# Optimization experiments

Measured on AMD Instinct MI355X. Metric: run time of the kernel, lower is better.

Reference implementation:

```python
import math
import jax, jax.numpy as jnp
import numpy as np

DIM = 2048
HEAD_DIM = 64
N_HEADS = DIM // HEAD_DIM
BATCH = 4
SEQ = 1025  # 32*32 axial positions + 1 zero position
EPS = 1e-6


def make_theta(head_dim=HEAD_DIM, h=32, w=32):
    # freqs: geometric from pi to 10*pi, head_dim//4 of them
    n_freqs = head_dim // 4
    freqs = jnp.exp(jnp.linspace(math.log(math.pi), math.log(10 * math.pi), n_freqs))
    hp = jnp.linspace(-1.0, 1.0, h + 1)
    wp = jnp.linspace(-1.0, 1.0, w + 1)
    hp = (hp[:-1] + hp[1:]) / 2
    wp = (wp[:-1] + wp[1:]) / 2
    pos = jnp.stack(jnp.meshgrid(hp, wp, indexing='ij'), axis=-1).reshape(h * w, 2)
    pos = jnp.concatenate([jnp.zeros((1, 2)), pos], axis=0)  # [1025, 2]
    theta_h = pos[:, 0:1] * freqs  # [S, n_freqs]
    theta_w = pos[:, 1:2] * freqs
    return jnp.concatenate([theta_h, theta_w], axis=-1)  # [S, head_dim//2]


def rms_norm(x, scale, eps=EPS):
    mean_sq = jnp.mean(jnp.square(x.astype(jnp.float32)), axis=-1, keepdims=True)
    s = scale.astype(jnp.float32) * jax.lax.rsqrt(mean_sq + eps)
    return (x * s.astype(x.dtype)).astype(x.dtype)


def apply_rotary(x, theta):
    # x: [B, H, S, D], theta: [S, d] with 2*d <= D
    d = theta.shape[-1]
    x1, x2, x3 = x[..., :d], x[..., d:2 * d], x[..., 2 * d:]
    cos, sin = jnp.cos(theta), jnp.sin(theta)  # broadcast over B, H
    y1 = x1 * cos - x2 * sin
    y2 = x2 * cos + x1 * sin
    return jnp.concatenate([y1, y2, x3], axis=-1)


def setup_inputs() -> dict:
    key = jax.random.key(0)
    k1, k2, k3 = jax.random.split(key, 3)
    x = jax.random.normal(k1, (BATCH, SEQ, DIM), dtype=jnp.float32)
    scale = jnp.ones((DIM,), dtype=jnp.float32)
    w_qkv = jax.random.normal(k2, (3 * DIM, DIM), dtype=jnp.float32) * 0.02
    w_out = jax.random.normal(k3, (DIM, DIM), dtype=jnp.float32) * 0.02
    return {"x": x, "scale": scale, "w_qkv": w_qkv, "w_out": w_out}


def reference(x, scale, w_qkv, w_out):
    B, S, _ = x.shape
    skip = x
    h = rms_norm(x, scale)
    qkv = h @ w_qkv.T  # [B, S, 3*DIM]
    qkv = qkv.reshape(B, S, 3, N_HEADS, HEAD_DIM)
    qkv = jnp.transpose(qkv, (0, 3, 2, 1, 4))  # [B, H, 3, S, D]
    q, k, v = qkv[:, :, 0], qkv[:, :, 1], qkv[:, :, 2]
    theta = make_theta()[:S]
    q = apply_rotary(q, theta)
    k = apply_rotary(k, theta)
    scores = jnp.einsum('bhqd,bhkd->bhqk', q, k) / math.sqrt(HEAD_DIM)
    causal = jnp.tril(jnp.ones((S, S), dtype=bool))
    scores = jnp.where(causal, scores, jnp.finfo(scores.dtype).min)
    attn = jax.nn.softmax(scores, axis=-1)
    o = jnp.einsum('bhqk,bhkd->bhqd', attn, v)  # [B, H, S, D]
    o = jnp.transpose(o, (0, 2, 1, 3)).reshape(B, S, DIM)
    return o @ w_out.T + skip
```

## Files before the change

### kernel.cpp

```cpp
#include <hip/hip_runtime.h>
#include <hip/hip_bf16.h>
#include <cstdint>

#define SEQ   1025
#define SPAD  1088
#define DIM   2048
#define NQKV  6144
#define MROWS 4100
#define MPAD  4352
#define NH    32

typedef __attribute__((ext_vector_type(8))) short bf16x8;
typedef __attribute__((ext_vector_type(4))) short bf16x4;
typedef __attribute__((ext_vector_type(4))) float f32x4;

#define MFMA16x16(A,B,C) __builtin_amdgcn_mfma_f32_16x16x32_bf16(A,B,C,0,0,0)

static __device__ __forceinline__ float bf2f(short s) {
    union { unsigned int u; float f; } v;
    v.u = ((unsigned int)(unsigned short)s) << 16;
    return v.f;
}
static __device__ __forceinline__ short f2bf(float f) {
    union { float f; unsigned int u; } v; v.f = f;
    unsigned int r = v.u + 0x7fffu + ((v.u >> 16) & 1u);
    return (short)(r >> 16);
}

typedef __attribute__((address_space(1))) unsigned int u32g;
typedef __attribute__((address_space(3))) unsigned int u32l;
static __device__ __forceinline__ void gld_lds16(void* lds, const void* g) {
    __builtin_amdgcn_global_load_lds((const u32g*)(uintptr_t)g,
                                     (u32l*)(uintptr_t)lds, 16, 0, 0);
}

#define SBX() __builtin_amdgcn_sched_barrier(0)
#define PRIO(x) __builtin_amdgcn_s_setprio(x)

__global__ __launch_bounds__(256) void trig_k(float* __restrict__ cosT, float* __restrict__ sinT) {
    int i = blockIdx.x * 256 + threadIdx.x;
    if (i >= SEQ * 16) return;
    int s = i >> 4, f = i & 15;
    float ph = 0.f, pw = 0.f;
    if (s > 0) {
        int p = s - 1;
        ph = -1.f + ((p >> 5) + 0.5f) * 0.0625f;
        pw = -1.f + ((p & 31) + 0.5f) * 0.0625f;
    }
    double fr = 3.141592653589793 * exp((double)f * 0.15350567286626973);
    float th = (float)(ph * fr), tw = (float)(pw * fr);
    cosT[s*32 + f]      = cosf(th);
    sinT[s*32 + f]      = sinf(th);
    cosT[s*32 + 16 + f] = cosf(tw);
    sinT[s*32 + 16 + f] = sinf(tw);
}

__global__ __launch_bounds__(256) void rmsnorm_k(const float* __restrict__ x,
                                                 const float* __restrict__ sc,
                                                 short* __restrict__ h) {
    int row = blockIdx.x, t = threadIdx.x;
    short* hr = h + (size_t)row * DIM;
    if (row >= MROWS) {
        bf16x8 z = {};
        *(bf16x8*)(hr + t*8) = z;
        return;
    }
    const float4* xr = (const float4*)(x + (size_t)row * DIM);
    float4 a = xr[2*t], b = xr[2*t+1];
    float ss = a.x*a.x + a.y*a.y + a.z*a.z + a.w*a.w
             + b.x*b.x + b.y*b.y + b.z*b.z + b.w*b.w;
    #pragma unroll
    for (int off = 32; off; off >>= 1) ss += __shfl_xor(ss, off, 64);
    __shared__ float red[4];
    if ((t & 63) == 0) red[t >> 6] = ss;
    __syncthreads();
    float ms = (red[0]+red[1]+red[2]+red[3]) * (1.0f/2048.0f);
    float inv = rsqrtf(ms + 1e-6f);
    const float4* sr = (const float4*)sc;
    float4 s0 = sr[2*t], s1 = sr[2*t+1];
    bf16x8 o;
    o[0]=f2bf(a.x*(s0.x*inv)); o[1]=f2bf(a.y*(s0.y*inv));
    o[2]=f2bf(a.z*(s0.z*inv)); o[3]=f2bf(a.w*(s0.w*inv));
    o[4]=f2bf(b.x*(s1.x*inv)); o[5]=f2bf(b.y*(s1.y*inv));
    o[6]=f2bf(b.z*(s1.z*inv)); o[7]=f2bf(b.w*(s1.w*inv));
    *(bf16x8*)(hr + t*8) = o;
}

__global__ __launch_bounds__(256) void conv_k(const float* __restrict__ in, short* __restrict__ o, int n4) {
    int i = blockIdx.x * 256 + threadIdx.x;
    if (i >= n4) return;
    float4 v = ((const float4*)in)[i];
    bf16x4 r = { f2bf(v.x), f2bf(v.y), f2bf(v.z), f2bf(v.w) };
    *(bf16x4*)(o + (size_t)i*4) = r;
}

template<int EPI>
__global__ __launch_bounds__(512, 2) void gemm8p(const short* __restrict__ A,
                                                 const short* __restrict__ B,
                                                 void* __restrict__ C,
                                                 const float* __restrict__ skip,
                                                 int N, int K, int nbm) {
    extern __shared__ char smem[];
    const int nwg = gridDim.x;
    const int cpx = nwg >> 3;
    const int bid = blockIdx.x;
    const int sid = (bid & 7) * cpx + (bid >> 3);
    const int bm = sid % nbm;
    const int bn = sid / nbm;

    const int t = threadIdx.x, w = t >> 6, l = t & 63;
    const int lr = l & 15, lg = l >> 4;
    const int wr = w >> 2, wc = w & 3;

    const short* Ab = A + (size_t)bm * 256 * K;
    const short* Bb = B + (size_t)bn * 256 * K;

    const int srow = t >> 3;
    const int scol = (((t & 7) ^ (srow & 7)) << 3);

    const int cs0 = (lg * 16) ^ ((lr & 7) << 4);
    const int cs1 = (64 + lg * 16) ^ ((lr & 7) << 4);
    const int aRowB = (wr * 128 + lr) * 128;
    const int bRowB = (wc * 64 + lr) * 128;

    f32x4 acc[8][4] = {};
    bf16x8 rA[4][2], rB[4][2];

#define STAGE8(kt, bb) do {                                                   \
    const int k0_ = (kt) * 64;                                                \
    _Pragma("unroll")                                                         \
    for (int c = 0; c < 4; ++c) {                                             \
        gld_lds16(smem + (bb)*65536 + c*8192 + (w<<10),                       \
                  Ab + (size_t)(c*64 + srow) * K + k0_ + scol);               \
        gld_lds16(smem + (bb)*65536 + 32768 + c*8192 + (w<<10),               \
                  Bb + (size_t)(c*64 + srow) * K + k0_ + scol);               \
    }                                                                         \
} while (0)

#define STAGE_P2(kt, bb) do {                                                 \
    const int k0_ = (kt) * 64;                                                \
    gld_lds16(smem + (bb)*65536 + 0*8192 + (w<<10),                           \
              Ab + (size_t)(0*64 + srow) * K + k0_ + scol);                   \
    gld_lds16(smem + (bb)*65536 + 2*8192 + (w<<10),                           \
              Ab + (size_t)(2*64 + srow) * K + k0_ + scol);                   \
    _Pragma("unroll")                                                         \
    for (int c = 0; c < 4; ++c)                                               \
        gld_lds16(smem + (bb)*65536 + 32768 + c*8192 + (w<<10),               \
                  Bb + (size_t)(c*64 + srow) * K + k0_ + scol);               \
} while (0)

#define STAGE_P3(kt, bb) do {                                                 \
    const int k0_ = (kt) * 64;                                                \
    gld_lds16(smem + (bb)*65536 + 1*8192 + (w<<10),                           \
              Ab + (size_t)(1*64 + srow) * K + k0_ + scol);                   \
    gld_lds16(smem + (bb)*65536 + 3*8192 + (w<<10),                           \
              Ab + (size_t)(3*64 + srow) * K + k0_ + scol);                   \
} while (0)

#define READ_A8(bb, h) do {                                                   \
    const char* p_ = smem + (bb)*65536 + aRowB + (h)*8192;                    \
    _Pragma("unroll")                                                         \
    for (int am = 0; am < 4; ++am) {                                          \
        rA[am][0] = *(const bf16x8*)(p_ + am*2048 + cs0);                     \
        rA[am][1] = *(const bf16x8*)(p_ + am*2048 + cs1);                     \
    }                                                                         \
} while (0)

#define READ_B4(bb, np) do {                                                  \
    const char* p_ = smem + (bb)*65536 + 32768 + bRowB + (np)*4096;           \
    _Pragma("unroll")                                                         \
    for (int nn = 0; nn < 2; ++nn) {                                          \
        rB[(np)*2+nn][0] = *(const bf16x8*)(p_ + nn*2048 + cs0);              \
        rB[(np)*2+nn][1] = *(const bf16x8*)(p_ + nn*2048 + cs1);              \
    }                                                                         \
} while (0)

#define MF_Q(h, nh) do {                                                      \
    _Pragma("unroll")                                                         \
    for (int am = 0; am < 4; ++am)                                            \
    _Pragma("unroll")                                                         \
    for (int nn = 0; nn < 2; ++nn) {                                          \
        acc[(h)*4+am][(nh)*2+nn] =                                            \
            MFMA16x16(rA[am][0], rB[(nh)*2+nn][0], acc[(h)*4+am][(nh)*2+nn]); \
        acc[(h)*4+am][(nh)*2+nn] =                                            \
            MFMA16x16(rA[am][1], rB[(nh)*2+nn][1], acc[(h)*4+am][(nh)*2+nn]); \
    }                                                                         \
} while (0)

#define BAR() do { SBX(); __builtin_amdgcn_s_barrier(); } while (0)

    STAGE8(0, 0);
    STAGE8(1, 1);
    asm volatile("s_waitcnt vmcnt(8)" ::: "memory"); SBX();
    __builtin_amdgcn_s_barrier();

    const int NT2 = K / 128;
    for (int it = 0; it < NT2; ++it) {
        const bool more = (it < NT2 - 1);
        READ_A8(0, 0); READ_B4(0, 0);
        PRIO(1); MF_Q(0, 0); PRIO(0); BAR();
        READ_B4(0, 1);
        PRIO(1); MF_Q(0, 1); PRIO(0); BAR();
        if (more) STAGE_P2(2*it + 2, 0);
        READ_A8(0, 1);
        PRIO(1); MF_Q(1, 1); PRIO(0); BAR();
        if (more) STAGE_P3(2*it + 2, 0);
        PRIO(1); MF_Q(1, 0); PRIO(0);
        if (more) { asm volatile("s_waitcnt vmcnt(8)" ::: "memory"); }
        else      { asm volatile("s_waitcnt vmcnt(0)" ::: "memory"); }
        BAR();
        READ_A8(1, 0); READ_B4(1, 0);
        PRIO(1); MF_Q(0, 0); PRIO(0); BAR();
        READ_B4(1, 1);
        PRIO(1); MF_Q(0, 1); PRIO(0); BAR();
        if (more) STAGE_P2(2*it + 3, 1);
        READ_A8(1, 1);
        PRIO(1); MF_Q(1, 1); PRIO(0); BAR();
        if (more) STAGE_P3(2*it + 3, 1);
        PRIO(1); MF_Q(1, 0); PRIO(0);
        if (more) { asm volatile("s_waitcnt vmcnt(8)" ::: "memory"); }
        BAR();
    }

    #pragma unroll
    for (int m = 0; m < 8; ++m) {
        const int row0 = bm*256 + wr*128 + m*16 + lg*4;
        #pragma unroll
        for (int n = 0; n < 4; ++n) {
            const int col = bn*256 + wc*64 + n*16 + lr;
            #pragma unroll
            for (int r = 0; r < 4; ++r) {
                const int row = row0 + r;
                if constexpr (EPI == 0) {
                    ((short*)C)[(size_t)row * N + col] = f2bf(acc[m][n][r]);
                } else {
                    if (row < MROWS)
                        ((float*)C)[(size_t)row * N + col] =
                            acc[m][n][r] + skip[(size_t)row * N + col];
                }
            }
        }
    }
#undef STAGE8
#undef STAGE_P2
#undef STAGE_P3
#undef READ_A8
#undef READ_B4
#undef MF_Q
#undef BAR
}

__global__ __launch_bounds__(256) void rearrange_k(const short* __restrict__ qkv,
        const float* __restrict__ cosT, const float* __restrict__ sinT,
        short* __restrict__ kr, short* __restrict__ vt) {
    int bid = blockIdx.x;
    int bh = bid / 17, st = bid % 17;
    int b = bh >> 5, hh = bh & 31;
    int s0 = st * 64;
    int t = threadIdx.x;
    __shared__ short vs[64][68];
    #pragma unroll
    for (int i = 0; i < 8; ++i) {
        int task = t + i*256;
        int sl = task >> 5, p = task & 31;
        int s = s0 + sl;
        float y1 = 0.f, y2 = 0.f;
        if (s < SEQ) {
            const short* src = qkv + (size_t)(b*SEQ + s)*NQKV + DIM + hh*64;
            float x1 = bf2f(src[p]), x2 = bf2f(src[32+p]);
            float c = cosT[s*32+p], sn = sinT[s*32+p];
            y1 = x1*c - x2*sn;
            y2 = x2*c + x1*sn;
        }
        short* dst = kr + ((size_t)bh*SPAD + s)*64;
        dst[p]    = f2bf(y1);
        dst[32+p] = f2bf(y2);
    }
    #pragma unroll
    for (int i = 0; i < 16; ++i) {
        int task = t + i*256;
        int sl = task >> 6, d = task & 63;
        int s = s0 + sl;
        short v = 0;
        if (s < SEQ) v = qkv[(size_t)(b*SEQ + s)*NQKV + 2*DIM + hh*64 + d];
        vs[sl][d] = v;
    }
    __syncthreads();
    #pragma unroll
    for (int i = 0; i < 16; ++i) {
        int task = t + i*256;
        int d = task >> 6, sl = task & 63;
        vt[((size_t)bh*64 + d)*SPAD + s0 + sl] = vs[sl][d];
    }
}

__global__ __launch_bounds__(256) void attn_k(const short* __restrict__ qkv,
        const short* __restrict__ kr, const short* __restrict__ vt,
        const float* __restrict__ cosT, const float* __restrict__ sinT,
        short* __restrict__ ob) {
    const int nwg = gridDim.x;
    const int cpx = nwg >> 3;
    const int bid = blockIdx.x;
    const int sid = (bid & 7) * cpx + (bid >> 3);
    const int bh = sid / 17;
    const int qt = sid % 17;
    const int q0 = qt * 64;
    const int b = bh >> 5, hh = bh & 31;
    const int t = threadIdx.x, w = t >> 6, l = t & 63;
    const int lr = l & 15, lg = l >> 4;

    __shared__ short Ks[64*64];
    __shared__ short Vts[64*64];

    const int qrow = q0 + w*16 + lr;
    const int qc = qrow < SEQ ? qrow : SEQ-1;
    const short* qsrc = qkv + (size_t)(b*SEQ + qc)*NQKV + hh*64;
    bf16x8 xlo = *(const bf16x8*)(qsrc + lg*8);
    bf16x8 xhi = *(const bf16x8*)(qsrc + 32 + lg*8);
    const float4* cp = (const float4*)(cosT + qc*32 + lg*8);
    const float4* sp = (const float4*)(sinT + qc*32 + lg*8);
    float cc[8], sn[8];
    { float4 u = cp[0], v2 = cp[1];
      cc[0]=u.x; cc[1]=u.y; cc[2]=u.z; cc[3]=u.w;
      cc[4]=v2.x; cc[5]=v2.y; cc[6]=v2.z; cc[7]=v2.w; }
    { float4 u = sp[0], v2 = sp[1];
      sn[0]=u.x; sn[1]=u.y; sn[2]=u.z; sn[3]=u.w;
      sn[4]=v2.x; sn[5]=v2.y; sn[6]=v2.z; sn[7]=v2.w; }
    bf16x8 qf0, qf1;
    #pragma unroll
    for (int j = 0; j < 8; ++j) {
        float x1 = bf2f(xlo[j]), x2 = bf2f(xhi[j]);
        qf0[j] = f2bf(x1*cc[j] - x2*sn[j]);
        qf1[j] = f2bf(x2*cc[j] + x1*sn[j]);
    }

    f32x4 oacc[4] = {};
    float mrun = -1e30f, lrun = 0.f;
    const int ntile = qt + 1;
    const float SC = 0.125f * 1.4426950408889634f;

    const char* kbase = (const char*)(kr + (size_t)bh * SPAD * 64);
    const char* vbase = (const char*)(vt + (size_t)bh * 64 * SPAD);
    const int srow8 = l >> 3;
    const int sslotB = ((l & 7) ^ srow8) << 4;
    const int swz = (lr & 7) << 4;

    for (int kt = 0; kt < ntile; ++kt) {
        const int kv0 = kt * 64;
        gld_lds16((char*)Ks + w*2048,
                  kbase + (size_t)(kv0 + w*16 + srow8)*128 + sslotB);
        gld_lds16((char*)Ks + w*2048 + 1024,
                  kbase + (size_t)(kv0 + w*16 + 8 + srow8)*128 + sslotB);
        gld_lds16((char*)Vts + w*2048,
                  vbase + (size_t)(w*16 + srow8)*(SPAD*2) + (size_t)kv0*2 + sslotB);
        gld_lds16((char*)Vts + w*2048 + 1024,
                  vbase + (size_t)(w*16 + 8 + srow8)*(SPAD*2) + (size_t)kv0*2 + sslotB);
        __syncthreads();

        f32x4 st[4];
        #pragma unroll
        for (int f = 0; f < 4; ++f) {
            const char* kp = (const char*)Ks + (f*16 + lr)*128;
            bf16x8 a0 = *(const bf16x8*)(kp + ((lg*16) ^ swz));
            bf16x8 a1 = *(const bf16x8*)(kp + ((64 + lg*16) ^ swz));
            f32x4 z = {};
            z = MFMA16x16(a0, qf0, z);
            st[f] = MFMA16x16(a1, qf1, z);
        }

        float pv[16];
        float tmax = -1e30f;
        #pragma unroll
        for (int f = 0; f < 4; ++f)
        #pragma unroll
        for (int r = 0; r < 4; ++r) {
            int kv = kv0 + f*16 + lg*4 + r;
            float v = st[f][r] * SC;
            v = (kv <= qrow && kv < SEQ) ? v : -1e30f;
            pv[f*4+r] = v; tmax = fmaxf(tmax, v);
        }
        tmax = fmaxf(tmax, __shfl_xor(tmax, 16, 64));
        tmax = fmaxf(tmax, __shfl_xor(tmax, 32, 64));
        float mnew = fmaxf(mrun, tmax);
        float alpha = exp2f(mrun - mnew);
        float psum = 0.f;
        bf16x8 pf0, pf1;
        #pragma unroll
        for (int j = 0; j < 4; ++j) {
            float p0 = exp2f(pv[0*4+j] - mnew);
            float p1 = exp2f(pv[1*4+j] - mnew);
            float p2 = exp2f(pv[2*4+j] - mnew);
            float p3 = exp2f(pv[3*4+j] - mnew);
            psum += (p0 + p1) + (p2 + p3);
            pf0[j] = f2bf(p0); pf0[4+j] = f2bf(p1);
            pf1[j] = f2bf(p2); pf1[4+j] = f2bf(p3);
        }
        psum += __shfl_xor(psum, 16, 64);
        psum += __shfl_xor(psum, 32, 64);
        lrun = lrun * alpha + psum;
        mrun = mnew;
        #pragma unroll
        for (int df = 0; df < 4; ++df) {
            oacc[df][0] *= alpha; oacc[df][1] *= alpha;
            oacc[df][2] *= alpha; oacc[df][3] *= alpha;
        }
        #pragma unroll
        for (int df = 0; df < 4; ++df) {
            const char* vp = (const char*)Vts + (df*16 + lr)*128;
            bf16x4 v0 = *(const bf16x4*)(vp + ((lg*8) ^ swz));
            bf16x4 v1 = *(const bf16x4*)(vp + ((32 + lg*8) ^ swz));
            bf16x4 v2 = *(const bf16x4*)(vp + ((64 + lg*8) ^ swz));
            bf16x4 v3 = *(const bf16x4*)(vp + ((96 + lg*8) ^ swz));
            bf16x8 vf0, vf1;
            vf0[0]=v0[0]; vf0[1]=v0[1]; vf0[2]=v0[2]; vf0[3]=v0[3];
            vf0[4]=v1[0]; vf0[5]=v1[1]; vf0[6]=v1[2]; vf0[7]=v1[3];
            vf1[0]=v2[0]; vf1[1]=v2[1]; vf1[2]=v2[2]; vf1[3]=v2[3];
            vf1[4]=v3[0]; vf1[5]=v3[1]; vf1[6]=v3[2]; vf1[7]=v3[3];
            oacc[df] = MFMA16x16(vf0, pf0, oacc[df]);
            oacc[df] = MFMA16x16(vf1, pf1, oacc[df]);
        }
        __syncthreads();
    }

    if (qrow < SEQ) {
        float inv = 1.0f / lrun;
        short* orow = ob + (size_t)(b*SEQ + qrow)*DIM + hh*64;
        #pragma unroll
        for (int df = 0; df < 4; ++df) {
            bf16x4 ov = { f2bf(oacc[df][0]*inv), f2bf(oacc[df][1]*inv),
                          f2bf(oacc[df][2]*inv), f2bf(oacc[df][3]*inv) };
            *(bf16x4*)(orow + df*16 + lg*4) = ov;
        }
    }
}

extern "C" void kernel_launch(void* const* d_in, const int* in_sizes, int n_in,
                              void* d_out, int out_size, void* d_ws, size_t ws_size,
                              hipStream_t stream) {
    const float* x     = (const float*)d_in[0];
    const float* scale = (const float*)d_in[1];
    const float* w_qkv = (const float*)d_in[2];
    const float* w_out = (const float*)d_in[3];
    float* out = (float*)d_out;

    char* ws = (char*)d_ws;
    size_t off = 0;
    auto alloc = [&](size_t bytes) -> char* {
        char* p = ws + off;
        off += (bytes + 255) & ~(size_t)255;
        return p;
    };
    float* cosT  = (float*)alloc((size_t)SEQ*32*4);
    float* sinT  = (float*)alloc((size_t)SEQ*32*4);
    short* h_b   = (short*)alloc((size_t)MPAD*DIM*2);
    short* wq_b  = (short*)alloc((size_t)NQKV*DIM*2);
    short* wo_b  = (short*)alloc((size_t)DIM*DIM*2);
    short* qkv_b = (short*)alloc((size_t)MPAD*NQKV*2);
    short* k_r   = (short*)alloc((size_t)128*SPAD*64*2);
    short* vt    = (short*)alloc((size_t)128*SPAD*64*2);
    short* o_b   = h_b;

    hipFuncSetAttribute((const void*)gemm8p<0>,
                        hipFuncAttributeMaxDynamicSharedMemorySize, 131072);
    hipFuncSetAttribute((const void*)gemm8p<1>,
                        hipFuncAttributeMaxDynamicSharedMemorySize, 131072);

    trig_k<<<65, 256, 0, stream>>>(cosT, sinT);
    rmsnorm_k<<<MPAD, 256, 0, stream>>>(x, scale, h_b);
    conv_k<<<(NQKV*DIM/4 + 255)/256, 256, 0, stream>>>(w_qkv, wq_b, NQKV*DIM/4);
    conv_k<<<(DIM*DIM/4 + 255)/256, 256, 0, stream>>>(w_out, wo_b, DIM*DIM/4);
    gemm8p<0><<<(MPAD/256)*(NQKV/256), 512, 131072, stream>>>(h_b, wq_b, qkv_b, nullptr, NQKV, DIM, MPAD/256);
    rearrange_k<<<128*17, 256, 0, stream>>>(qkv_b, cosT, sinT, k_r, vt);
    attn_k<<<17*128, 256, 0, stream>>>(qkv_b, k_r, vt, cosT, sinT, o_b);
    gemm8p<1><<<(MPAD/256)*(DIM/256), 512, 131072, stream>>>(o_b, wo_b, out, x, DIM, DIM, MPAD/256);
}
```

Before: 436.5 us.

## Reschedule GEMM staging, double-buffer attention K/V, merge weight conversion kernels

The GEMM main loop is restructured so A and B halves are staged separately into LDS and interleaved with MFMA quarters. Explicit waitcnt and barrier pairs bracket each quarter, with B fragments split into two register arrays. The attention kernel double-buffers its K/V tiles so the next tile's loads overlap the current tile's compute. The two weight-conversion launches are merged into one kernel. Together these aim to hide load latency and cut launch overhead, at the cost of delicate manual synchronisation and twice the attention LDS.

```diff
diff --git a/kernel.cpp b/kernel.cpp
--- a/kernel.cpp
+++ b/kernel.cpp
@@ -36,6 +36,8 @@
 
 #define SBX() __builtin_amdgcn_sched_barrier(0)
 #define PRIO(x) __builtin_amdgcn_s_setprio(x)
+#define VMCNT(n) asm volatile("s_waitcnt vmcnt(" #n ")" ::: "memory")
+#define LGKM(n)  asm volatile("s_waitcnt lgkmcnt(" #n ")" ::: "memory")
 
 __global__ __launch_bounds__(256) void trig_k(float* __restrict__ cosT, float* __restrict__ sinT) {
     int i = blockIdx.x * 256 + threadIdx.x;
@@ -86,12 +88,15 @@
     *(bf16x8*)(hr + t*8) = o;
 }
 
-__global__ __launch_bounds__(256) void conv_k(const float* __restrict__ in, short* __restrict__ o, int n4) {
+__global__ __launch_bounds__(256) void conv2_k(const float* __restrict__ a, short* __restrict__ oa, int n4a,
+                                               const float* __restrict__ b, short* __restrict__ ob, int n4b) {
     int i = blockIdx.x * 256 + threadIdx.x;
-    if (i >= n4) return;
-    float4 v = ((const float4*)in)[i];
+    const float* src; short* dst; int j;
+    if (i < n4a) { src = a; dst = oa; j = i; }
+    else { j = i - n4a; if (j >= n4b) return; src = b; dst = ob; }
+    float4 v = ((const float4*)src)[j];
     bf16x4 r = { f2bf(v.x), f2bf(v.y), f2bf(v.z), f2bf(v.w) };
-    *(bf16x4*)(o + (size_t)i*4) = r;
+    *(bf16x4*)(dst + (size_t)j*4) = r;
 }
 
 template<int EPI>
@@ -120,45 +125,30 @@
 
     const int cs0 = (lg * 16) ^ ((lr & 7) << 4);
     const int cs1 = (64 + lg * 16) ^ ((lr & 7) << 4);
-    const int aRowB = (wr * 128 + lr) * 128;
-    const int bRowB = (wc * 64 + lr) * 128;
+    const int aBase = wr * 16384 + lr * 128;
+    const int bBase = 32768 + (wc >> 1) * 16384 + ((wc & 1) * 64 + lr) * 128;
 
     f32x4 acc[8][4] = {};
-    bf16x8 rA[4][2], rB[4][2];
-
-#define STAGE8(kt, bb) do {                                                   \
+    bf16x8 rA[4][2], rB01[2][2], rB23[2][2];
+
+#define STAGE_A(kt, half, bb) do {                                            \
     const int k0_ = (kt) * 64;                                                \
-    _Pragma("unroll")                                                         \
-    for (int c = 0; c < 4; ++c) {                                             \
-        gld_lds16(smem + (bb)*65536 + c*8192 + (w<<10),                       \
-                  Ab + (size_t)(c*64 + srow) * K + k0_ + scol);               \
-        gld_lds16(smem + (bb)*65536 + 32768 + c*8192 + (w<<10),               \
-                  Bb + (size_t)(c*64 + srow) * K + k0_ + scol);               \
-    }                                                                         \
-} while (0)
-
-#define STAGE_P2(kt, bb) do {                                                 \
+    gld_lds16(smem + (bb)*65536 + (half)*16384 + (w<<10),                     \
+              Ab + (size_t)((half)*128 + srow) * K + k0_ + scol);             \
+    gld_lds16(smem + (bb)*65536 + (half)*16384 + 8192 + (w<<10),              \
+              Ab + (size_t)((half)*128 + 64 + srow) * K + k0_ + scol);        \
+} while (0)
+
+#define STAGE_B(kt, half, bb) do {                                            \
     const int k0_ = (kt) * 64;                                                \
-    gld_lds16(smem + (bb)*65536 + 0*8192 + (w<<10),                           \
-              Ab + (size_t)(0*64 + srow) * K + k0_ + scol);                   \
-    gld_lds16(smem + (bb)*65536 + 2*8192 + (w<<10),                           \
-              Ab + (size_t)(2*64 + srow) * K + k0_ + scol);                   \
-    _Pragma("unroll")                                                         \
-    for (int c = 0; c < 4; ++c)                                               \
-        gld_lds16(smem + (bb)*65536 + 32768 + c*8192 + (w<<10),               \
-                  Bb + (size_t)(c*64 + srow) * K + k0_ + scol);               \
-} while (0)
-
-#define STAGE_P3(kt, bb) do {                                                 \
-    const int k0_ = (kt) * 64;                                                \
-    gld_lds16(smem + (bb)*65536 + 1*8192 + (w<<10),                           \
-              Ab + (size_t)(1*64 + srow) * K + k0_ + scol);                   \
-    gld_lds16(smem + (bb)*65536 + 3*8192 + (w<<10),                           \
-              Ab + (size_t)(3*64 + srow) * K + k0_ + scol);                   \
-} while (0)
-
-#define READ_A8(bb, h) do {                                                   \
-    const char* p_ = smem + (bb)*65536 + aRowB + (h)*8192;                    \
+    gld_lds16(smem + (bb)*65536 + 32768 + (half)*16384 + (w<<10),             \
+              Bb + (size_t)((half)*128 + srow) * K + k0_ + scol);             \
+    gld_lds16(smem + (bb)*65536 + 32768 + (half)*16384 + 8192 + (w<<10),      \
+              Bb + (size_t)((half)*128 + 64 + srow) * K + k0_ + scol);        \
+} while (0)
+
+#define READ_A(bb, h) do {                                                    \
+    const char* p_ = smem + (bb)*65536 + aBase + (h)*8192;                    \
     _Pragma("unroll")                                                         \
     for (int am = 0; am < 4; ++am) {                                          \
         rA[am][0] = *(const bf16x8*)(p_ + am*2048 + cs0);                     \
@@ -166,60 +156,68 @@
     }                                                                         \
 } while (0)
 
-#define READ_B4(bb, np) do {                                                  \
-    const char* p_ = smem + (bb)*65536 + 32768 + bRowB + (np)*4096;           \
+#define READ_B(bb, np, arr) do {                                              \
+    const char* p_ = smem + (bb)*65536 + bBase + (np)*4096;                   \
     _Pragma("unroll")                                                         \
     for (int nn = 0; nn < 2; ++nn) {                                          \
-        rB[(np)*2+nn][0] = *(const bf16x8*)(p_ + nn*2048 + cs0);              \
-        rB[(np)*2+nn][1] = *(const bf16x8*)(p_ + nn*2048 + cs1);              \
+        arr[nn][0] = *(const bf16x8*)(p_ + nn*2048 + cs0);                    \
+        arr[nn][1] = *(const bf16x8*)(p_ + nn*2048 + cs1);                    \
     }                                                                         \
 } while (0)
 
-#define MF_Q(h, nh) do {                                                      \
+#define MF_Q(h, np, arr) do {                                                 \
     _Pragma("unroll")                                                         \
     for (int am = 0; am < 4; ++am)                                            \
     _Pragma("unroll")                                                         \
     for (int nn = 0; nn < 2; ++nn) {                                          \
-        acc[(h)*4+am][(nh)*2+nn] =                                            \
-            MFMA16x16(rA[am][0], rB[(nh)*2+nn][0], acc[(h)*4+am][(nh)*2+nn]); \
-        acc[(h)*4+am][(nh)*2+nn] =                                            \
-            MFMA16x16(rA[am][1], rB[(nh)*2+nn][1], acc[(h)*4+am][(nh)*2+nn]); \
+        acc[(h)*4+am][(np)*2+nn] =                                            \
+            MFMA16x16(rA[am][0], arr[nn][0], acc[(h)*4+am][(np)*2+nn]);       \
+        acc[(h)*4+am][(np)*2+nn] =                                            \
+            MFMA16x16(rA[am][1], arr[nn][1], acc[(h)*4+am][(np)*2+nn]);       \
     }                                                                         \
 } while (0)
 
-#define BAR() do { SBX(); __builtin_amdgcn_s_barrier(); } while (0)
-
-    STAGE8(0, 0);
-    STAGE8(1, 1);
-    asm volatile("s_waitcnt vmcnt(8)" ::: "memory"); SBX();
-    __builtin_amdgcn_s_barrier();
+#define BOPEN()  do { SBX(); __builtin_amdgcn_s_barrier(); LGKM(0); SBX(); } while (0)
+#define BOPEN_NL() do { SBX(); __builtin_amdgcn_s_barrier(); SBX(); } while (0)
+#define BCLOSE() do { SBX(); __builtin_amdgcn_s_barrier(); SBX(); } while (0)
+
+    STAGE_B(0, 0, 0); STAGE_B(0, 1, 0);
+    STAGE_A(0, 0, 0); STAGE_A(0, 1, 0);
+    STAGE_B(1, 0, 1); STAGE_B(1, 1, 1);
+    VMCNT(4); SBX();
+    __builtin_amdgcn_s_barrier(); SBX();
 
     const int NT2 = K / 128;
     for (int it = 0; it < NT2; ++it) {
         const bool more = (it < NT2 - 1);
-        READ_A8(0, 0); READ_B4(0, 0);
-        PRIO(1); MF_Q(0, 0); PRIO(0); BAR();
-        READ_B4(0, 1);
-        PRIO(1); MF_Q(0, 1); PRIO(0); BAR();
-        if (more) STAGE_P2(2*it + 2, 0);
-        READ_A8(0, 1);
-        PRIO(1); MF_Q(1, 1); PRIO(0); BAR();
-        if (more) STAGE_P3(2*it + 2, 0);
-        PRIO(1); MF_Q(1, 0); PRIO(0);
-        if (more) { asm volatile("s_waitcnt vmcnt(8)" ::: "memory"); }
-        else      { asm volatile("s_waitcnt vmcnt(0)" ::: "memory"); }
-        BAR();
-        READ_A8(1, 0); READ_B4(1, 0);
-        PRIO(1); MF_Q(0, 0); PRIO(0); BAR();
-        READ_B4(1, 1);
-        PRIO(1); MF_Q(0, 1); PRIO(0); BAR();
-        if (more) STAGE_P2(2*it + 3, 1);
-        READ_A8(1, 1);
-        PRIO(1); MF_Q(1, 1); PRIO(0); BAR();
-        if (more) STAGE_P3(2*it + 3, 1);
-        PRIO(1); MF_Q(1, 0); PRIO(0);
-        if (more) { asm volatile("s_waitcnt vmcnt(8)" ::: "memory"); }
-        BAR();
+        READ_A(0, 0); READ_B(0, 0, rB01);
+        STAGE_A(2*it + 1, 0, 1);
+        LGKM(8);
+        BOPEN(); PRIO(1); MF_Q(0, 0, rB01); PRIO(0); BCLOSE();
+        READ_B(0, 1, rB23);
+        STAGE_A(2*it + 1, 1, 1);
+        BOPEN(); PRIO(1); MF_Q(0, 1, rB23); PRIO(0); BCLOSE();
+        READ_A(0, 1);
+        if (more) STAGE_B(2*it + 2, 0, 0);
+        BOPEN(); PRIO(1); MF_Q(1, 1, rB23); PRIO(0); BCLOSE();
+        if (more) STAGE_B(2*it + 2, 1, 0);
+        BOPEN_NL(); PRIO(1); MF_Q(1, 0, rB01); PRIO(0); SBX();
+        if (more) { VMCNT(4); } else { VMCNT(0); }
+        BCLOSE();
+        READ_A(1, 0); READ_B(1, 0, rB01);
+        if (more) STAGE_A(2*it + 2, 0, 0);
+        LGKM(8);
+        BOPEN(); PRIO(1); MF_Q(0, 0, rB01); PRIO(0); BCLOSE();
+        READ_B(1, 1, rB23);
+        if (more) STAGE_A(2*it + 2, 1, 0);
+        BOPEN(); PRIO(1); MF_Q(0, 1, rB23); PRIO(0); BCLOSE();
+        READ_A(1, 1);
+        if (more) STAGE_B(2*it + 3, 0, 1);
+        BOPEN(); PRIO(1); MF_Q(1, 1, rB23); PRIO(0); BCLOSE();
+        if (more) STAGE_B(2*it + 3, 1, 1);
+        BOPEN_NL(); PRIO(1); MF_Q(1, 0, rB01); PRIO(0); SBX();
+        if (more) { VMCNT(4); }
+        BCLOSE();
     }
 
     #pragma unroll
@@ -241,13 +239,14 @@
             }
         }
     }
-#undef STAGE8
-#undef STAGE_P2
-#undef STAGE_P3
-#undef READ_A8
-#undef READ_B4
+#undef STAGE_A
+#undef STAGE_B
+#undef READ_A
+#undef READ_B
 #undef MF_Q
-#undef BAR
+#undef BOPEN
+#undef BOPEN_NL
+#undef BCLOSE
 }
 
 __global__ __launch_bounds__(256) void rearrange_k(const short* __restrict__ qkv,
@@ -309,8 +308,8 @@
     const int t = threadIdx.x, w = t >> 6, l = t & 63;
     const int lr = l & 15, lg = l >> 4;
 
-    __shared__ short Ks[64*64];
-    __shared__ short Vts[64*64];
+    __shared__ short Ks[2][64*64];
+    __shared__ short Vts[2][64*64];
 
     const int qrow = q0 + w*16 + lr;
     const int qc = qrow < SEQ ? qrow : SEQ-1;
@@ -345,22 +344,31 @@
     const int sslotB = ((l & 7) ^ srow8) << 4;
     const int swz = (lr & 7) << 4;
 
+#define STAGE_KV(kt, c) do {                                                   \
+    const int kv0_ = (kt) * 64;                                                \
+    gld_lds16((char*)Ks[c] + w*2048,                                           \
+              kbase + (size_t)(kv0_ + w*16 + srow8)*128 + sslotB);             \
+    gld_lds16((char*)Ks[c] + w*2048 + 1024,                                    \
+              kbase + (size_t)(kv0_ + w*16 + 8 + srow8)*128 + sslotB);         \
+    gld_lds16((char*)Vts[c] + w*2048,                                          \
+              vbase + (size_t)(w*16 + srow8)*(SPAD*2) + (size_t)kv0_*2 + sslotB); \
+    gld_lds16((char*)Vts[c] + w*2048 + 1024,                                   \
+              vbase + (size_t)(w*16 + 8 + srow8)*(SPAD*2) + (size_t)kv0_*2 + sslotB); \
+} while (0)
+
+    STAGE_KV(0, 0);
+
     for (int kt = 0; kt < ntile; ++kt) {
         const int kv0 = kt * 64;
-        gld_lds16((char*)Ks + w*2048,
-                  kbase + (size_t)(kv0 + w*16 + srow8)*128 + sslotB);
-        gld_lds16((char*)Ks + w*2048 + 1024,
-                  kbase + (size_t)(kv0 + w*16 + 8 + srow8)*128 + sslotB);
-        gld_lds16((char*)Vts + w*2048,
-                  vbase + (size_t)(w*16 + srow8)*(SPAD*2) + (size_t)kv0*2 + sslotB);
-        gld_lds16((char*)Vts + w*2048 + 1024,
-                  vbase + (size_t)(w*16 + 8 + srow8)*(SPAD*2) + (size_t)kv0*2 + sslotB);
-        __syncthreads();
+        const int cur = kt & 1;
+        if (kt + 1 < ntile) { STAGE_KV(kt + 1, cur ^ 1); SBX(); VMCNT(4); }
+        else { SBX(); VMCNT(0); }
+        SBX(); __builtin_amdgcn_s_barrier(); SBX();
 
         f32x4 st[4];
         #pragma unroll
         for (int f = 0; f < 4; ++f) {
-            const char* kp = (const char*)Ks + (f*16 + lr)*128;
+            const char* kp = (const char*)Ks[cur] + (f*16 + lr)*128;
             bf16x8 a0 = *(const bf16x8*)(kp + ((lg*16) ^ swz));
             bf16x8 a1 = *(const bf16x8*)(kp + ((64 + lg*16) ^ swz));
             f32x4 z = {};
@@ -406,7 +414,7 @@
         }
         #pragma unroll
         for (int df = 0; df < 4; ++df) {
-            const char* vp = (const char*)Vts + (df*16 + lr)*128;
+            const char* vp = (const char*)Vts[cur] + (df*16 + lr)*128;
             bf16x4 v0 = *(const bf16x4*)(vp + ((lg*8) ^ swz));
             bf16x4 v1 = *(const bf16x4*)(vp + ((32 + lg*8) ^ swz));
             bf16x4 v2 = *(const bf16x4*)(vp + ((64 + lg*8) ^ swz));
@@ -419,8 +427,9 @@
             oacc[df] = MFMA16x16(vf0, pf0, oacc[df]);
             oacc[df] = MFMA16x16(vf1, pf1, oacc[df]);
         }
-        __syncthreads();
-    }
+        SBX(); __builtin_amdgcn_s_barrier(); SBX();
+    }
+#undef STAGE_KV
 
     if (qrow < SEQ) {
         float inv = 1.0f / lrun;
@@ -467,8 +476,8 @@
 
     trig_k<<<65, 256, 0, stream>>>(cosT, sinT);
     rmsnorm_k<<<MPAD, 256, 0, stream>>>(x, scale, h_b);
-    conv_k<<<(NQKV*DIM/4 + 255)/256, 256, 0, stream>>>(w_qkv, wq_b, NQKV*DIM/4);
-    conv_k<<<(DIM*DIM/4 + 255)/256, 256, 0, stream>>>(w_out, wo_b, DIM*DIM/4);
+    conv2_k<<<(NQKV*DIM/4 + DIM*DIM/4 + 255)/256, 256, 0, stream>>>(
+        w_qkv, wq_b, NQKV*DIM/4, w_out, wo_b, DIM*DIM/4);
     gemm8p<0><<<(MPAD/256)*(NQKV/256), 512, 131072, stream>>>(h_b, wq_b, qkv_b, nullptr, NQKV, DIM, MPAD/256);
     rearrange_k<<<128*17, 256, 0, stream>>>(qkv_b, cosT, sinT, k_r, vt);
     attn_k<<<17*128, 256, 0, stream>>>(qkv_b, k_r, vt, cosT, sinT, o_b);
```

Result: no change. 440.1 us (+0.8%).
